# Optimization experiments

Hardware: AMD Instinct MI355X
Metric: run time of the kernel (lower is better)

## Reference

```python
import jax, jax.numpy as jnp
import numpy as np

N_HEAD, D_MODEL, D_K, D_V = 16, 1024, 64, 64
BATCH, SEQ = 4, 2048


def setup_inputs() -> dict:
    key = jax.random.key(0)
    ks = jax.random.split(key, 9)
    s = 1.0 / np.sqrt(D_MODEL)
    so = 1.0 / np.sqrt(N_HEAD * D_V)
    inp = {
        "input": jax.random.normal(ks[0], (BATCH, SEQ, D_MODEL), jnp.float32),
        # causal mask: True => masked (set to -inf), matching masked_fill semantics
        "attn_mask": jnp.triu(jnp.ones((SEQ, SEQ), bool), k=1),
        "Wq": jax.random.uniform(ks[1], (D_MODEL, N_HEAD * D_K), jnp.float32, -s, s),
        "bq": jax.random.uniform(ks[2], (N_HEAD * D_K,), jnp.float32, -s, s),
        "Wk": jax.random.uniform(ks[3], (D_MODEL, N_HEAD * D_K), jnp.float32, -s, s),
        "bk": jax.random.uniform(ks[4], (N_HEAD * D_K,), jnp.float32, -s, s),
        "Wv": jax.random.uniform(ks[5], (D_MODEL, N_HEAD * D_V), jnp.float32, -s, s),
        "bv": jax.random.uniform(ks[6], (N_HEAD * D_V,), jnp.float32, -s, s),
        "Wo": jax.random.uniform(ks[7], (N_HEAD * D_V, D_MODEL), jnp.float32, -so, so),
        "bo": jax.random.uniform(ks[8], (D_MODEL,), jnp.float32, -so, so),
    }
    return inp


def reference(input, attn_mask, Wq, bq, Wk, bk, Wv, bv, Wo, bo):
    B, S, _ = input.shape
    scale = 1.0 / np.sqrt(D_K)
    q = (input @ Wq + bq).reshape(B, S, N_HEAD, D_K)  # bshd
    k = (input @ Wk + bk).reshape(B, S, N_HEAD, D_K)
    v = (input @ Wv + bv).reshape(B, S, N_HEAD, D_V)
    # scores [B, H, S, S]
    score = jnp.einsum("bqhd,bkhd->bhqk", q, k) * scale
    score = jnp.where(attn_mask[None, None], -jnp.inf, score)
    prob = jax.nn.softmax(score, axis=-1)
    attn = jnp.einsum("bhqk,bkhd->bqhd", prob, v).reshape(B, S, N_HEAD * D_V)
    return attn @ Wo + bo
```

## Files before the change

### kernel.cpp

```cpp
#include <hip/hip_runtime.h>
#include <math.h>


typedef __attribute__((ext_vector_type(8))) short short8;
typedef __attribute__((ext_vector_type(4))) short s16x4;
typedef __attribute__((ext_vector_type(4))) float f32x4;
typedef __attribute__((ext_vector_type(4))) unsigned short u16x4;
typedef __attribute__((ext_vector_type(2))) unsigned int u32x2;

constexpr int B  = 4;
constexpr int S  = 2048;
constexpr int H  = 16;
constexpr int DM = 1024;
constexpr int M  = B * S;

__device__ __forceinline__ unsigned short f2bf(float f) {
    union { float f; unsigned u; } v; v.f = f;
    unsigned r = v.u + 0x7FFFu + ((v.u >> 16) & 1u);
    return (unsigned short)(r >> 16);
}

__device__ __forceinline__ s16x4 pack_bf16x4(float a, float b, float c, float d) {
    unsigned r0, r1;
    asm("v_cvt_pk_bf16_f32 %0, %1, %2" : "=v"(r0) : "v"(a), "v"(b));
    asm("v_cvt_pk_bf16_f32 %0, %1, %2" : "=v"(r1) : "v"(c), "v"(d));
    u32x2 t; t[0] = r0; t[1] = r1;
    return __builtin_bit_cast(s16x4, t);
}

__device__ __forceinline__ void gload16(const void* g, void* l) {
    __builtin_amdgcn_global_load_lds(
        (const __attribute__((address_space(1))) void*)g,
        (__attribute__((address_space(3))) void*)l, 16, 0, 0);
}

__device__ __forceinline__ f32x4 mfma_16x16x16(s16x4 a, s16x4 b, f32x4 c) {
#if __has_builtin(__builtin_amdgcn_mfma_f32_16x16x16bf16_1k)
    return __builtin_amdgcn_mfma_f32_16x16x16bf16_1k(a, b, c, 0, 0, 0);
#else
    asm("v_mfma_f32_16x16x16_bf16 %0, %1, %2, %0" : "+v"(c) : "v"(a), "v"(b));
    return c;
#endif
}

__global__ __launch_bounds__(256) void cast_x_kernel(
    const float* __restrict__ in, unsigned short* __restrict__ out)
{
    const size_t i = (size_t)blockIdx.x * 256 + threadIdx.x;
    const float4* p = (const float4*)in;
    float4 a = p[2 * i], b = p[2 * i + 1];
    short8 o;
    o[0] = (short)f2bf(a.x); o[1] = (short)f2bf(a.y);
    o[2] = (short)f2bf(a.z); o[3] = (short)f2bf(a.w);
    o[4] = (short)f2bf(b.x); o[5] = (short)f2bf(b.y);
    o[6] = (short)f2bf(b.z); o[7] = (short)f2bf(b.w);
    *(short8*)(out + 8 * i) = o;
}

__global__ __launch_bounds__(256) void transpose_cast_w(
    const float* __restrict__ W0, const float* __restrict__ W1,
    const float* __restrict__ W2, const float* __restrict__ W3,
    unsigned short* __restrict__ T0, unsigned short* __restrict__ T1,
    unsigned short* __restrict__ T2, unsigned short* __restrict__ T3)
{
    const int z = blockIdx.z;
    const float* W = (z == 0) ? W0 : (z == 1) ? W1 : (z == 2) ? W2 : W3;
    unsigned short* Wt = (z == 0) ? T0 : (z == 1) ? T1 : (z == 2) ? T2 : T3;

    __shared__ float tile[32][33];
    const int t = threadIdx.x;
    const int r0 = blockIdx.y * 32, c0 = blockIdx.x * 32;
    {
        const int r = t >> 3, c4 = (t & 7) * 4;
        float4 a = *(const float4*)&W[(size_t)(r0 + r) * 1024 + c0 + c4];
        tile[r][c4 + 0] = a.x; tile[r][c4 + 1] = a.y;
        tile[r][c4 + 2] = a.z; tile[r][c4 + 3] = a.w;
    }
    __syncthreads();
    {
        const int n = t >> 3, k4 = (t & 7) * 4;
        u16x4 o;
        o[0] = f2bf(tile[k4 + 0][n]); o[1] = f2bf(tile[k4 + 1][n]);
        o[2] = f2bf(tile[k4 + 2][n]); o[3] = f2bf(tile[k4 + 3][n]);
        *(u16x4*)&Wt[(size_t)(c0 + n) * 1024 + r0 + k4] = o;
    }
}

template <int FUSED>
__global__ __launch_bounds__(256) void gemm_bf16(
    const unsigned short* __restrict__ X, const unsigned short* __restrict__ Wt,
    const float* __restrict__ bias_q, const float* __restrict__ bias_k,
    const float* __restrict__ bias_v,
    void* __restrict__ dq, void* __restrict__ dk, void* __restrict__ dv,
    float qscale)
{
    constexpr int GX  = (FUSED == 1) ? 24 : 8;
    constexpr int NWG = GX * 64;

    __shared__ __align__(16) unsigned short As[2][128 * 32];
    __shared__ __align__(16) unsigned short Bs[2][128 * 32];

    const int t = threadIdx.x;
    const int lane = t & 63, w = t >> 6;
    const int wr = w >> 1, wc = w & 1;
    const int l15 = lane & 15, lhi = lane >> 4;

    const int L = blockIdx.x;
    const int orig = (L & 7) * (NWG / 8) + (L >> 3);
    const int row0 = (orig / GX) * 128, col0 = (orig % GX) * 128;

    const f32x4 z = {0.f, 0.f, 0.f, 0.f};
    f32x4 acc[4][4];
    #pragma unroll
    for (int i = 0; i < 4; ++i)
        #pragma unroll
        for (int j = 0; j < 4; ++j) acc[i][j] = z;

    const int fchunk = ((lhi ^ ((l15 >> 1) & 3)) << 4);

    auto STAGE = [&](int buf, int k0) {
        #pragma unroll
        for (int i = 0; i < 2; ++i) {
            int seg = t + i * 256;
            int row = seg >> 2;
            int ch  = (seg & 3) ^ ((row >> 1) & 3);
            gload16(X  + (size_t)(row0 + row) * 1024 + k0 + ch * 8,
                    (char*)As[buf] + seg * 16);
            gload16(Wt + (size_t)(col0 + row) * 1024 + k0 + ch * 8,
                    (char*)Bs[buf] + seg * 16);
        }
    };

    STAGE(0, 0);
    for (int k0 = 0; k0 < 1024; k0 += 32) {
        const int cur = (k0 >> 5) & 1;
        __syncthreads();
        if (k0 + 32 < 1024) STAGE(cur ^ 1, k0 + 32);

        short8 a[4], b[4];
        #pragma unroll
        for (int mi = 0; mi < 4; ++mi)
            a[mi] = *(const short8*)((const char*)As[cur]
                + (wr * 64 + mi * 16 + l15) * 64 + fchunk);
        #pragma unroll
        for (int ni = 0; ni < 4; ++ni)
            b[ni] = *(const short8*)((const char*)Bs[cur]
                + (wc * 64 + ni * 16 + l15) * 64 + fchunk);
        #pragma unroll
        for (int mi = 0; mi < 4; ++mi)
            #pragma unroll
            for (int ni = 0; ni < 4; ++ni)
                acc[mi][ni] = __builtin_amdgcn_mfma_f32_16x16x32_bf16(
                    a[mi], b[ni], acc[mi][ni], 0, 0, 0);
    }

    #pragma unroll
    for (int mi = 0; mi < 4; ++mi)
        #pragma unroll
        for (int ni = 0; ni < 4; ++ni) {
            const int cc = col0 + wc * 64 + ni * 16 + l15;
            if constexpr (FUSED == 1) {
                const int sel = cc >> 10;
                const int hh = (cc >> 6) & 15, dd = cc & 63;
                const float bv = (sel == 0 ? bias_q : sel == 1 ? bias_k : bias_v)
                                 [cc & 1023];
                const int rr0 = row0 + wr * 64 + mi * 16 + lhi * 4;
                const int b0i = rr0 >> 11, s0_ = rr0 & 2047;
                if (sel == 2) {
                    const int sstore = s0_ ^ (((cc >> 3) & 1) << 2);
                    s16x4 pv = pack_bf16x4(
                        acc[mi][ni][0] + bv, acc[mi][ni][1] + bv,
                        acc[mi][ni][2] + bv, acc[mi][ni][3] + bv);
                    *(s16x4*)&((unsigned short*)dv)[
                        (((size_t)(b0i * 16 + hh) * 64 + dd) << 11) + sstore] = pv;
                } else {
                    unsigned short* dst = (unsigned short*)(sel == 0 ? dq : dk);
                    const float sc_ = (sel == 0) ? qscale : 1.0f;
                    #pragma unroll
                    for (int r = 0; r < 4; ++r)
                        dst[(((size_t)(b0i * 16 + hh) * 2048 + s0_ + r) << 6) + dd]
                            = f2bf((acc[mi][ni][r] + bv) * sc_);
                }
            } else {
                const float bv = bias_q[cc];
                #pragma unroll
                for (int r = 0; r < 4; ++r) {
                    const int rr = row0 + wr * 64 + mi * 16 + lhi * 4 + r;
                    ((float*)dq)[(size_t)rr * 1024 + cc] = acc[mi][ni][r] + bv;
                }
            }
        }
}

__global__ __launch_bounds__(256) void attn_mfma(
    const unsigned short* __restrict__ Q, const unsigned short* __restrict__ K,
    const unsigned short* __restrict__ Vt, unsigned short* __restrict__ Out)
{
    __shared__ __align__(16) unsigned short Ks[2][64 * 64];
    __shared__ __align__(16) unsigned short Vs[2][64 * 64];

    const int t = threadIdx.x, lane = t & 63, w = t >> 6;
    const int l15 = lane & 15, lhi = lane >> 4;
    const int id = blockIdx.x;
    const int j = id >> 6;
    const int bx = (j < 8) ? j : 15 - (j & 7);
    const int bh = id & 63;
    const int q0 = bx * 128;
    const size_t base = (size_t)bh * S * 64;

    short8 bq[2][2];
    #pragma unroll
    for (int mi = 0; mi < 2; ++mi)
        #pragma unroll
        for (int ks = 0; ks < 2; ++ks)
            bq[mi][ks] = *(const short8*)(Q + base
                + (size_t)(q0 + w * 32 + mi * 16 + l15) * 64 + ks * 32 + lhi * 8);

    const f32x4 z = {0.f, 0.f, 0.f, 0.f};
    f32x4 o[2][4];
    float mrow[2] = {-INFINITY, -INFINITY}, lrow[2] = {0.f, 0.f};
    #pragma unroll
    for (int mi = 0; mi < 2; ++mi)
        #pragma unroll
        for (int d = 0; d < 4; ++d) o[mi][d] = z;

    auto STAGE = [&](int buf, int kt) {
        const int k0 = kt * 64;
        #pragma unroll
        for (int i = 0; i < 2; ++i) {
            int seg = t + i * 256;
            int row = seg >> 3;
            int ch  = (seg & 7) ^ (row & 7);
            gload16(K + base + (size_t)(k0 + row) * 64 + ch * 8,
                    (char*)Ks[buf] + seg * 16);
            gload16(Vt + ((size_t)bh * 64 + row) * S + k0 + ch * 8,
                    (char*)Vs[buf] + seg * 16);
        }
    };

    const int ntiles = 2 * bx + 2;
    STAGE(0, 0);
    __syncthreads();

    for (int kt = 0; kt < ntiles; ++kt) {
        const int cur = kt & 1;
        const int k0 = kt * 64;
        if (kt + 1 < ntiles) STAGE(cur ^ 1, kt + 1);

        f32x4 sc[2][4];
        #pragma unroll
        for (int mi = 0; mi < 2; ++mi)
            #pragma unroll
            for (int ni = 0; ni < 4; ++ni) sc[mi][ni] = z;
        __builtin_amdgcn_s_setprio(1);
        #pragma unroll
        for (int ks = 0; ks < 2; ++ks)
            #pragma unroll
            for (int ni = 0; ni < 4; ++ni) {
                short8 ak = *(const short8*)((const char*)Ks[cur]
                    + (ni * 16 + l15) * 128 + (((ks * 4 + lhi) ^ (l15 & 7)) << 4));
                #pragma unroll
                for (int mi = 0; mi < 2; ++mi)
                    sc[mi][ni] = __builtin_amdgcn_mfma_f32_16x16x32_bf16(
                        ak, bq[mi][ks], sc[mi][ni], 0, 0, 0);
            }
        __builtin_amdgcn_s_setprio(0);

        if (k0 >= q0) {
            #pragma unroll
            for (int mi = 0; mi < 2; ++mi) {
                const int qg = q0 + w * 32 + mi * 16 + l15;
                #pragma unroll
                for (int ni = 0; ni < 4; ++ni)
                    #pragma unroll
                    for (int r = 0; r < 4; ++r)
                        if (k0 + ni * 16 + lhi * 4 + r > qg)
                            sc[mi][ni][r] = -INFINITY;
            }
        }

        s16x4 pf[2][4];
        #pragma unroll
        for (int mi = 0; mi < 2; ++mi) {
            float tm = -INFINITY;
            #pragma unroll
            for (int ni = 0; ni < 4; ++ni) {
                float a0 = fmaxf(sc[mi][ni][0], sc[mi][ni][1]);
                float a1 = fmaxf(sc[mi][ni][2], sc[mi][ni][3]);
                tm = fmaxf(tm, fmaxf(a0, a1));
            }
            tm = fmaxf(tm, __shfl_xor(tm, 16));
            tm = fmaxf(tm, __shfl_xor(tm, 32));
            if (!__all(tm <= mrow[mi] + 8.f)) {
                const float mnew = fmaxf(mrow[mi], tm);
                const float alpha = exp2f(mrow[mi] - mnew);
                mrow[mi] = mnew;
                lrow[mi] *= alpha;
                #pragma unroll
                for (int d = 0; d < 4; ++d) {
                    o[mi][d][0] *= alpha; o[mi][d][1] *= alpha;
                    o[mi][d][2] *= alpha; o[mi][d][3] *= alpha;
                }
            }
            float ps = 0.f;
            #pragma unroll
            for (int ni = 0; ni < 4; ++ni) {
                float p0 = exp2f(sc[mi][ni][0] - mrow[mi]);
                float p1 = exp2f(sc[mi][ni][1] - mrow[mi]);
                float p2 = exp2f(sc[mi][ni][2] - mrow[mi]);
                float p3 = exp2f(sc[mi][ni][3] - mrow[mi]);
                ps += (p0 + p1) + (p2 + p3);
                pf[mi][ni] = pack_bf16x4(p0, p1, p2, p3);
            }
            ps += __shfl_xor(ps, 16);
            ps += __shfl_xor(ps, 32);
            lrow[mi] += ps;
        }

        __builtin_amdgcn_s_setprio(1);
        #pragma unroll
        for (int ni = 0; ni < 4; ++ni) {
            #pragma unroll
            for (int db = 0; db < 4; ++db) {
                const int row = db * 16 + l15;
                const int slot = ((ni * 2 + (lhi >> 1)) ^ (l15 & 7));
                const int half = (lhi & 1) ^ ((l15 >> 3) & 1);
                s16x4 av = *(const s16x4*)((const char*)Vs[cur]
                    + row * 128 + slot * 16 + half * 8);
                #pragma unroll
                for (int mi = 0; mi < 2; ++mi)
                    o[mi][db] = mfma_16x16x16(av, pf[mi][ni], o[mi][db]);
            }
        }
        __builtin_amdgcn_s_setprio(0);

        __syncthreads();
    }

    const int b_ = bh >> 4, h_ = bh & 15;
    #pragma unroll
    for (int mi = 0; mi < 2; ++mi) {
        const float inv = 1.0f / lrow[mi];
        const int s_ = q0 + w * 32 + mi * 16 + l15;
        #pragma unroll
        for (int db = 0; db < 4; ++db) {
            s16x4 ov = pack_bf16x4(o[mi][db][0] * inv, o[mi][db][1] * inv,
                                   o[mi][db][2] * inv, o[mi][db][3] * inv);
            *(s16x4*)&Out[(size_t)(b_ * S + s_) * 1024 + h_ * 64 + db * 16 + lhi * 4]
                = ov;
        }
    }
}

extern "C" void kernel_launch(void* const* d_in, const int* in_sizes, int n_in,
                              void* d_out, int out_size, void* d_ws, size_t ws_size,
                              hipStream_t stream)
{
    const float* x  = (const float*)d_in[0];
    const float* Wq = (const float*)d_in[2];
    const float* bq = (const float*)d_in[3];
    const float* Wk = (const float*)d_in[4];
    const float* bk = (const float*)d_in[5];
    const float* Wv = (const float*)d_in[6];
    const float* bv = (const float*)d_in[7];
    const float* Wo = (const float*)d_in[8];
    const float* bo = (const float*)d_in[9];
    float* out = (float*)d_out;

    unsigned short* p = (unsigned short*)d_ws;
    unsigned short* xb  = p; p += (size_t)M * DM;
    unsigned short* wqt = p; p += (size_t)DM * DM;
    unsigned short* wkt = p; p += (size_t)DM * DM;
    unsigned short* wvt = p; p += (size_t)DM * DM;
    unsigned short* wot = p; p += (size_t)DM * DM;
    unsigned short* qb  = p; p += (size_t)M * DM;
    unsigned short* kb  = p; p += (size_t)M * DM;
    unsigned short* vtb = p; p += (size_t)M * DM;
    unsigned short* attnb = p;

    cast_x_kernel<<<M * DM / 8 / 256, 256, 0, stream>>>(x, xb);
    transpose_cast_w<<<dim3(32, 32, 4), 256, 0, stream>>>(
        Wq, Wk, Wv, Wo, wqt, wkt, wvt, wot);

    const float qscale = 0.125f * 1.44269504088896340736f;
    gemm_bf16<1><<<dim3(24 * 64), 256, 0, stream>>>(
        xb, wqt, bq, bk, bv, qb, kb, vtb, qscale);

    attn_mfma<<<dim3(1024), 256, 0, stream>>>(qb, kb, vtb, attnb);

    gemm_bf16<0><<<dim3(8 * 64), 256, 0, stream>>>(
        attnb, wot, bo, nullptr, nullptr, out, nullptr, nullptr, 1.0f);
}
```

Before: 296.0 us.

## Stage Q/K epilogue through LDS for coalesced stores; halve output GEMM tile

The QKV GEMM epilogue for Q and K now writes bf16 results into the shared-memory A/B buffers with a swizzle, then copies them out with 16-byte coalesced stores per head row, replacing scattered 2-byte global stores. The output projection becomes its own kernel with a 64x128 tile and 1024 workgroups instead of 512 at 128x128, to improve occupancy and load balance across CUs. The costs are extra LDS traffic and syncs in the epilogue, and lower per-block reuse in the output GEMM.

```diff
diff --git a/kernel.cpp b/kernel.cpp
--- a/kernel.cpp
+++ b/kernel.cpp
@@ -86,15 +86,14 @@
     }
 }
 
-template <int FUSED>
-__global__ __launch_bounds__(256) void gemm_bf16(
+__global__ __launch_bounds__(256) void gemm_qkv(
     const unsigned short* __restrict__ X, const unsigned short* __restrict__ Wt,
     const float* __restrict__ bias_q, const float* __restrict__ bias_k,
     const float* __restrict__ bias_v,
-    void* __restrict__ dq, void* __restrict__ dk, void* __restrict__ dv,
-    float qscale)
-{
-    constexpr int GX  = (FUSED == 1) ? 24 : 8;
+    unsigned short* __restrict__ dq, unsigned short* __restrict__ dk,
+    unsigned short* __restrict__ dv, float qscale)
+{
+    constexpr int GX  = 24;
     constexpr int NWG = GX * 64;
 
     __shared__ __align__(16) unsigned short As[2][128 * 32];
@@ -154,40 +153,139 @@
                     a[mi], b[ni], acc[mi][ni], 0, 0, 0);
     }
 
-    #pragma unroll
-    for (int mi = 0; mi < 4; ++mi)
+    const int sel = col0 >> 10;
+    const int b0i = row0 >> 11, s0_ = row0 & 2047;
+
+    if (sel == 2) {
+        #pragma unroll
+        for (int mi = 0; mi < 4; ++mi)
+            #pragma unroll
+            for (int ni = 0; ni < 4; ++ni) {
+                const int cc = col0 + wc * 64 + ni * 16 + l15;
+                const int hh = (cc >> 6) & 15, dd = cc & 63;
+                const float bv = bias_v[cc & 1023];
+                const int sr = s0_ + wr * 64 + mi * 16 + lhi * 4;
+                const int sstore = sr ^ (((cc >> 3) & 1) << 2);
+                s16x4 pv = pack_bf16x4(
+                    acc[mi][ni][0] + bv, acc[mi][ni][1] + bv,
+                    acc[mi][ni][2] + bv, acc[mi][ni][3] + bv);
+                *(s16x4*)&dv[(((size_t)(b0i * 16 + hh) * 64 + dd) << 11) + sstore] = pv;
+            }
+    } else {
+        const float* bias = (sel == 0) ? bias_q : bias_k;
+        const float scl = (sel == 0) ? qscale : 1.0f;
+        unsigned short* dst = (sel == 0) ? dq : dk;
+        const int cb = (col0 & 1023) + wc * 64;
+        unsigned short* bounce = (wc == 0) ? (unsigned short*)As
+                                           : (unsigned short*)Bs;
+        __syncthreads();
+        #pragma unroll
+        for (int mi = 0; mi < 4; ++mi)
+            #pragma unroll
+            for (int ni = 0; ni < 4; ++ni) {
+                const float bv = bias[cb + ni * 16 + l15];
+                const int e0 = (wr * 64 + mi * 16 + lhi * 4) * 64
+                             + ((ni ^ lhi) * 16 + l15);
+                #pragma unroll
+                for (int r = 0; r < 4; ++r)
+                    bounce[e0 + r * 64] = f2bf((acc[mi][ni][r] + bv) * scl);
+            }
+        __syncthreads();
+        const unsigned short* src = (w < 2) ? (const unsigned short*)As
+                                            : (const unsigned short*)Bs;
+        const int head = ((col0 + ((w < 2) ? 0 : 64)) >> 6) & 15;
+        const size_t gbase = ((size_t)(b0i * 16 + head) * 2048 + s0_) * 64;
+        const int t2 = t & 127;
+        #pragma unroll
+        for (int p = 0; p < 8; ++p) {
+            const int idx = t2 + p * 128;
+            const int row = idx >> 3, c = idx & 7;
+            const int cs = c ^ (((row >> 2) & 3) << 1);
+            short8 vv = *(const short8*)&src[row * 64 + cs * 8];
+            *(short8*)&dst[gbase + (size_t)row * 64 + c * 8] = vv;
+        }
+    }
+}
+
+__global__ __launch_bounds__(256) void gemm_out(
+    const unsigned short* __restrict__ X, const unsigned short* __restrict__ Wt,
+    const float* __restrict__ bias, float* __restrict__ out)
+{
+    constexpr int GX  = 8;
+    constexpr int NWG = 128 * GX;
+
+    __shared__ __align__(16) unsigned short As[2][64 * 32];
+    __shared__ __align__(16) unsigned short Bs[2][128 * 32];
+
+    const int t = threadIdx.x;
+    const int lane = t & 63, w = t >> 6;
+    const int wr = w >> 1, wc = w & 1;
+    const int l15 = lane & 15, lhi = lane >> 4;
+
+    const int L = blockIdx.x;
+    const int orig = (L & 7) * (NWG / 8) + (L >> 3);
+    const int row0 = (orig / GX) * 64, col0 = (orig % GX) * 128;
+
+    const f32x4 z = {0.f, 0.f, 0.f, 0.f};
+    f32x4 acc[2][4];
+    #pragma unroll
+    for (int i = 0; i < 2; ++i)
+        #pragma unroll
+        for (int j = 0; j < 4; ++j) acc[i][j] = z;
+
+    const int fchunk = ((lhi ^ ((l15 >> 1) & 3)) << 4);
+
+    auto STAGE = [&](int buf, int k0) {
+        {
+            int seg = t;
+            int row = seg >> 2;
+            int ch  = (seg & 3) ^ ((row >> 1) & 3);
+            gload16(X + (size_t)(row0 + row) * 1024 + k0 + ch * 8,
+                    (char*)As[buf] + seg * 16);
+        }
+        #pragma unroll
+        for (int i = 0; i < 2; ++i) {
+            int seg = t + i * 256;
+            int row = seg >> 2;
+            int ch  = (seg & 3) ^ ((row >> 1) & 3);
+            gload16(Wt + (size_t)(col0 + row) * 1024 + k0 + ch * 8,
+                    (char*)Bs[buf] + seg * 16);
+        }
+    };
+
+    STAGE(0, 0);
+    for (int k0 = 0; k0 < 1024; k0 += 32) {
+        const int cur = (k0 >> 5) & 1;
+        __syncthreads();
+        if (k0 + 32 < 1024) STAGE(cur ^ 1, k0 + 32);
+
+        short8 a[2], b[4];
+        #pragma unroll
+        for (int mi = 0; mi < 2; ++mi)
+            a[mi] = *(const short8*)((const char*)As[cur]
+                + (wr * 32 + mi * 16 + l15) * 64 + fchunk);
+        #pragma unroll
+        for (int ni = 0; ni < 4; ++ni)
+            b[ni] = *(const short8*)((const char*)Bs[cur]
+                + (wc * 64 + ni * 16 + l15) * 64 + fchunk);
+        #pragma unroll
+        for (int mi = 0; mi < 2; ++mi)
+            #pragma unroll
+            for (int ni = 0; ni < 4; ++ni)
+                acc[mi][ni] = __builtin_amdgcn_mfma_f32_16x16x32_bf16(
+                    a[mi], b[ni], acc[mi][ni], 0, 0, 0);
+    }
+
+    #pragma unroll
+    for (int mi = 0; mi < 2; ++mi)
         #pragma unroll
         for (int ni = 0; ni < 4; ++ni) {
             const int cc = col0 + wc * 64 + ni * 16 + l15;
-            if constexpr (FUSED == 1) {
-                const int sel = cc >> 10;
-                const int hh = (cc >> 6) & 15, dd = cc & 63;
-                const float bv = (sel == 0 ? bias_q : sel == 1 ? bias_k : bias_v)
-                                 [cc & 1023];
-                const int rr0 = row0 + wr * 64 + mi * 16 + lhi * 4;
-                const int b0i = rr0 >> 11, s0_ = rr0 & 2047;
-                if (sel == 2) {
-                    const int sstore = s0_ ^ (((cc >> 3) & 1) << 2);
-                    s16x4 pv = pack_bf16x4(
-                        acc[mi][ni][0] + bv, acc[mi][ni][1] + bv,
-                        acc[mi][ni][2] + bv, acc[mi][ni][3] + bv);
-                    *(s16x4*)&((unsigned short*)dv)[
-                        (((size_t)(b0i * 16 + hh) * 64 + dd) << 11) + sstore] = pv;
-                } else {
-                    unsigned short* dst = (unsigned short*)(sel == 0 ? dq : dk);
-                    const float sc_ = (sel == 0) ? qscale : 1.0f;
-                    #pragma unroll
-                    for (int r = 0; r < 4; ++r)
-                        dst[(((size_t)(b0i * 16 + hh) * 2048 + s0_ + r) << 6) + dd]
-                            = f2bf((acc[mi][ni][r] + bv) * sc_);
-                }
-            } else {
-                const float bv = bias_q[cc];
-                #pragma unroll
-                for (int r = 0; r < 4; ++r) {
-                    const int rr = row0 + wr * 64 + mi * 16 + lhi * 4 + r;
-                    ((float*)dq)[(size_t)rr * 1024 + cc] = acc[mi][ni][r] + bv;
-                }
+            const float bv = bias[cc];
+            #pragma unroll
+            for (int r = 0; r < 4; ++r) {
+                const int rr = row0 + wr * 32 + mi * 16 + lhi * 4 + r;
+                out[(size_t)rr * 1024 + cc] = acc[mi][ni][r] + bv;
             }
         }
 }
@@ -383,11 +481,10 @@
         Wq, Wk, Wv, Wo, wqt, wkt, wvt, wot);
 
     const float qscale = 0.125f * 1.44269504088896340736f;
-    gemm_bf16<1><<<dim3(24 * 64), 256, 0, stream>>>(
+    gemm_qkv<<<dim3(24 * 64), 256, 0, stream>>>(
         xb, wqt, bq, bk, bv, qb, kb, vtb, qscale);
 
     attn_mfma<<<dim3(1024), 256, 0, stream>>>(qb, kb, vtb, attnb);
 
-    gemm_bf16<0><<<dim3(8 * 64), 256, 0, stream>>>(
-        attnb, wot, bo, nullptr, nullptr, out, nullptr, nullptr, 1.0f);
-}
+    gemm_out<<<dim3(1024), 256, 0, stream>>>(attnb, wot, bo, out);
+}
```

New measurement: 317.5 us. 7.3% more time.
